# Kernel tuning notes

Hardware: AMD Instinct MI355X
Metric: run time of the kernel (lower is better)

Reference implementation:

```python
import jax, jax.numpy as jnp
import numpy as np

COST_CLASS, COST_BBOX, COST_GIOU = 2.0, 5.0, 2.0
ALPHA, GAMMA, EPS = 0.25, 2.0, 1e-8


def _cxcywh_to_xyxy(b):
    cx, cy, w, h = b[..., 0], b[..., 1], b[..., 2], b[..., 3]
    return jnp.stack([cx - 0.5 * w, cy - 0.5 * h, cx + 0.5 * w, cy + 0.5 * h], axis=-1)


def _generalized_box_iou(boxes1, boxes2):
    # boxes1: [N,4], boxes2: [T,4] in xyxy -> [N,T]
    area1 = (boxes1[:, 2] - boxes1[:, 0]) * (boxes1[:, 3] - boxes1[:, 1])
    area2 = (boxes2[:, 2] - boxes2[:, 0]) * (boxes2[:, 3] - boxes2[:, 1])
    lt = jnp.maximum(boxes1[:, None, :2], boxes2[None, :, :2])
    rb = jnp.minimum(boxes1[:, None, 2:], boxes2[None, :, 2:])
    wh = jnp.clip(rb - lt, 0.0)
    inter = wh[..., 0] * wh[..., 1]
    union = area1[:, None] + area2[None, :] - inter
    iou = inter / union
    lt_e = jnp.minimum(boxes1[:, None, :2], boxes2[None, :, :2])
    rb_e = jnp.maximum(boxes1[:, None, 2:], boxes2[None, :, 2:])
    wh_e = jnp.clip(rb_e - lt_e, 0.0)
    area_e = wh_e[..., 0] * wh_e[..., 1]
    return iou - (area_e - union) / area_e


def setup_inputs() -> dict:
    key = jax.random.key(0)
    k1, k2, k3, k4 = jax.random.split(key, 4)
    bs, nq, nc, T = 16, 900, 91, 1600
    pred_logits = jax.random.normal(k1, (bs, nq, nc), dtype=jnp.float32)
    pred_boxes = jax.random.uniform(k2, (bs, nq, 4), dtype=jnp.float32)
    tgt_ids = jax.random.randint(k3, (T,), 0, nc, dtype=jnp.int64) if jax.config.jax_enable_x64 else jax.random.randint(k3, (T,), 0, nc, dtype=jnp.int32)
    tgt_bbox = jax.random.uniform(k4, (T, 4), dtype=jnp.float32)
    return {"pred_logits": pred_logits, "pred_boxes": pred_boxes,
            "tgt_ids": tgt_ids, "tgt_bbox": tgt_bbox}


def reference(pred_logits, pred_boxes, tgt_ids, tgt_bbox):
    bs, nq, nc = pred_logits.shape
    out_prob = jax.nn.sigmoid(pred_logits.reshape(bs * nq, nc))  # [N, C]
    out_bbox = pred_boxes.reshape(bs * nq, 4)                    # [N, 4]

    # -GIoU cost
    cost_giou = -_generalized_box_iou(_cxcywh_to_xyxy(out_bbox), _cxcywh_to_xyxy(tgt_bbox))

    # focal-style classification cost (alpha/gamma hardcoded in the source forward)
    neg_cost_class = (1.0 - ALPHA) * out_prob ** GAMMA * (-jnp.log(1.0 - out_prob + EPS))
    pos_cost_class = ALPHA * (1.0 - out_prob) ** GAMMA * (-jnp.log(out_prob + EPS))
    cost_class = pos_cost_class[:, tgt_ids] - neg_cost_class[:, tgt_ids]  # [N, T]

    # L1 cdist between box vectors
    cost_bbox = jnp.sum(jnp.abs(out_bbox[:, None, :] - tgt_bbox[None, :, :]), axis=-1)

    C = COST_BBOX * cost_bbox + COST_CLASS * cost_class + COST_GIOU * cost_giou
    return C.reshape(bs, nq, -1)
```

## Files before the change

### kernel.cpp

```cpp
#include <hip/hip_runtime.h>


#define NC 91
#define TT 1600
#define T4 (TT / 4)
#define ROWS 8
#define NTHREADS 448

typedef float vfloat4 __attribute__((ext_vector_type(4)));

__global__ __launch_bounds__(NTHREADS) void matcher_kernel(
    const float* __restrict__ logits,
    const float4* __restrict__ pboxes,
    const int4* __restrict__ tids,
    const float4* __restrict__ tboxes,
    vfloat4* __restrict__ out)
{
    __shared__ float tab[ROWS][NC];

    const int n0 = blockIdx.x * ROWS;
    const int tid = threadIdx.x;

    for (int i = tid; i < ROWS * NC; i += NTHREADS) {
        const int r = i / NC, c = i - r * NC;
        const float x = logits[(size_t)(n0 + r) * NC + c];
        const float p = __builtin_amdgcn_rcpf(1.f + __expf(-x));
        const float omp = 1.f - p;
        const float neg = 0.75f * p * p * (-__logf(omp + 1e-8f));
        const float pos = 0.25f * omp * omp * (-__logf(p + 1e-8f));
        tab[r][c] = 2.f * (pos - neg) + 2.f;
    }
    __syncthreads();

    const int t4 = tid;
    if (t4 < T4) {
        const int4 ids = tids[t4];
        const int idv[4] = {ids.x, ids.y, ids.z, ids.w};
        float tx0[4], ty0[4], tx1[4], ty1[4], ta[4], tcx[4], tcy[4], tw[4], th[4];
#pragma unroll
        for (int j = 0; j < 4; ++j) {
            const float4 b = tboxes[t4 * 4 + j];
            tcx[j] = b.x; tcy[j] = b.y; tw[j] = b.z; th[j] = b.w;
            tx0[j] = b.x - 0.5f * b.z;
            ty0[j] = b.y - 0.5f * b.w;
            tx1[j] = b.x + 0.5f * b.z;
            ty1[j] = b.y + 0.5f * b.w;
            ta[j] = b.z * b.w;
        }
#pragma unroll
        for (int r = 0; r < ROWS; ++r) {
            const float4 b = pboxes[n0 + r];
            const float pcx = b.x, pcy = b.y, pw = b.z, ph = b.w;
            const float px0 = pcx - 0.5f * pw, py0 = pcy - 0.5f * ph;
            const float px1 = pcx + 0.5f * pw, py1 = pcy + 0.5f * ph;
            const float pa  = pw * ph;
            vfloat4 res;
#pragma unroll
            for (int j = 0; j < 4; ++j) {
                const float iwr = fminf(px1, tx1[j]) - fmaxf(px0, tx0[j]);
                const float ihr = fminf(py1, ty1[j]) - fmaxf(py0, ty0[j]);
                const float inter = fmaxf(iwr, 0.f) * fmaxf(ihr, 0.f);
                const float uni = pa + ta[j] - inter;
                const float ew = (pw + tw[j]) - iwr;
                const float eh = (ph + th[j]) - ihr;
                const float ae = ew * eh;
                const float l1 = fabsf(pcx - tcx[j]) + fabsf(pcy - tcy[j])
                               + fabsf(pw - tw[j]) + fabsf(ph - th[j]);
                res[j] = 5.f * l1 + tab[r][idv[j]]
                       - 2.f * inter * __builtin_amdgcn_rcpf(uni)
                       - 2.f * uni * __builtin_amdgcn_rcpf(ae);
            }
            __builtin_nontemporal_store(res, &out[(size_t)(n0 + r) * T4 + t4]);
        }
    }
}

extern "C" void kernel_launch(void* const* d_in, const int* in_sizes, int n_in,
                              void* d_out, int out_size, void* d_ws, size_t ws_size,
                              hipStream_t stream) {
    const float* logits  = (const float*)d_in[0];
    const float4* pboxes = (const float4*)d_in[1];
    const int4* tids     = (const int4*)d_in[2];
    const float4* tboxes = (const float4*)d_in[3];
    vfloat4* out = (vfloat4*)d_out;
    const int N = in_sizes[1] / 4;
    matcher_kernel<<<N / ROWS, NTHREADS, 0, stream>>>(logits, pboxes, tids, tboxes, out);
}
```

Measured before the change: 123.2 us.

## Prefetch target data before logits table, trim target registers, raise occupancy

Target ids and boxes are now loaded before the logits-table build, so their global latency overlaps the transcendental work and the barrier. Only the four xyxy corners per target are kept in registers, and width, height and center are recomputed inside the inner loop, which lowers register pressure. A minimum of 7 blocks per CU is added to the launch bounds. Output stores become regular stores instead of nontemporal ones, which may change how the large output stream interacts with the cache.

Result: slower. 134.1 us (+8.8%).

```diff
diff --git a/kernel.cpp b/kernel.cpp
--- a/kernel.cpp
+++ b/kernel.cpp
@@ -9,7 +9,7 @@
 
 typedef float vfloat4 __attribute__((ext_vector_type(4)));
 
-__global__ __launch_bounds__(NTHREADS) void matcher_kernel(
+__global__ __launch_bounds__(NTHREADS, 7) void matcher_kernel(
     const float* __restrict__ logits,
     const float4* __restrict__ pboxes,
     const int4* __restrict__ tids,
@@ -20,6 +20,15 @@
 
     const int n0 = blockIdx.x * ROWS;
     const int tid = threadIdx.x;
+    const bool active = (tid < T4);
+
+    int4 ids = {0, 0, 0, 0};
+    float4 tb[4];
+    if (active) {
+        ids = tids[tid];
+#pragma unroll
+        for (int j = 0; j < 4; ++j) tb[j] = tboxes[tid * 4 + j];
+    }
 
     for (int i = tid; i < ROWS * NC; i += NTHREADS) {
         const int r = i / NC, c = i - r * NC;
@@ -32,46 +41,46 @@
     }
     __syncthreads();
 
-    const int t4 = tid;
-    if (t4 < T4) {
-        const int4 ids = tids[t4];
-        const int idv[4] = {ids.x, ids.y, ids.z, ids.w};
-        float tx0[4], ty0[4], tx1[4], ty1[4], ta[4], tcx[4], tcy[4], tw[4], th[4];
+    if (!active) return;
+
+    const int idv[4] = {ids.x, ids.y, ids.z, ids.w};
+    float tx0[4], ty0[4], tx1[4], ty1[4];
+#pragma unroll
+    for (int j = 0; j < 4; ++j) {
+        tx0[j] = tb[j].x - 0.5f * tb[j].z;
+        ty0[j] = tb[j].y - 0.5f * tb[j].w;
+        tx1[j] = tb[j].x + 0.5f * tb[j].z;
+        ty1[j] = tb[j].y + 0.5f * tb[j].w;
+    }
+
+#pragma unroll
+    for (int r = 0; r < ROWS; ++r) {
+        const float4 b = pboxes[n0 + r];
+        const float pcx = b.x, pcy = b.y, pw = b.z, ph = b.w;
+        const float px0 = pcx - 0.5f * pw, py0 = pcy - 0.5f * ph;
+        const float px1 = pcx + 0.5f * pw, py1 = pcy + 0.5f * ph;
+        const float pa  = pw * ph;
+        vfloat4 res;
 #pragma unroll
         for (int j = 0; j < 4; ++j) {
-            const float4 b = tboxes[t4 * 4 + j];
-            tcx[j] = b.x; tcy[j] = b.y; tw[j] = b.z; th[j] = b.w;
-            tx0[j] = b.x - 0.5f * b.z;
-            ty0[j] = b.y - 0.5f * b.w;
-            tx1[j] = b.x + 0.5f * b.z;
-            ty1[j] = b.y + 0.5f * b.w;
-            ta[j] = b.z * b.w;
+            const float tw = tx1[j] - tx0[j];
+            const float th = ty1[j] - ty0[j];
+            const float iwr = fminf(px1, tx1[j]) - fmaxf(px0, tx0[j]);
+            const float ihr = fminf(py1, ty1[j]) - fmaxf(py0, ty0[j]);
+            const float inter = fmaxf(iwr, 0.f) * fmaxf(ihr, 0.f);
+            const float uni = pa + tw * th - inter;
+            const float ew = (pw + tw) - iwr;
+            const float eh = (ph + th) - ihr;
+            const float ae = ew * eh;
+            const float tcx = tx0[j] + 0.5f * tw;
+            const float tcy = ty0[j] + 0.5f * th;
+            const float l1 = fabsf(pcx - tcx) + fabsf(pcy - tcy)
+                           + fabsf(pw - tw) + fabsf(ph - th);
+            res[j] = 5.f * l1 + tab[r][idv[j]]
+                   - 2.f * inter * __builtin_amdgcn_rcpf(uni)
+                   - 2.f * uni * __builtin_amdgcn_rcpf(ae);
         }
-#pragma unroll
-        for (int r = 0; r < ROWS; ++r) {
-            const float4 b = pboxes[n0 + r];
-            const float pcx = b.x, pcy = b.y, pw = b.z, ph = b.w;
-            const float px0 = pcx - 0.5f * pw, py0 = pcy - 0.5f * ph;
-            const float px1 = pcx + 0.5f * pw, py1 = pcy + 0.5f * ph;
-            const float pa  = pw * ph;
-            vfloat4 res;
-#pragma unroll
-            for (int j = 0; j < 4; ++j) {
-                const float iwr = fminf(px1, tx1[j]) - fmaxf(px0, tx0[j]);
-                const float ihr = fminf(py1, ty1[j]) - fmaxf(py0, ty0[j]);
-                const float inter = fmaxf(iwr, 0.f) * fmaxf(ihr, 0.f);
-                const float uni = pa + ta[j] - inter;
-                const float ew = (pw + tw[j]) - iwr;
-                const float eh = (ph + th[j]) - ihr;
-                const float ae = ew * eh;
-                const float l1 = fabsf(pcx - tcx[j]) + fabsf(pcy - tcy[j])
-                               + fabsf(pw - tw[j]) + fabsf(ph - th[j]);
-                res[j] = 5.f * l1 + tab[r][idv[j]]
-                       - 2.f * inter * __builtin_amdgcn_rcpf(uni)
-                       - 2.f * uni * __builtin_amdgcn_rcpf(ae);
-            }
-            __builtin_nontemporal_store(res, &out[(size_t)(n0 + r) * T4 + t4]);
-        }
+        out[(size_t)(n0 + r) * T4 + tid] = res;
     }
 }
 
```
